# Performance work log

Measured on AMD Instinct MI355X. Metric: run time of the kernel, lower is better.

Reference implementation:

```python
import jax, jax.numpy as jnp
import numpy as np

B, S, D_MODEL, N_HEADS = 4, 2048, 1024, 16
HEAD_DIM = D_MODEL // N_HEADS


def setup_inputs() -> dict:
    key = jax.random.key(0)
    k_x, k_wqkv, k_bqkv, k_wout, k_bout = jax.random.split(key, 5)
    x = jax.random.normal(k_x, (B, S, D_MODEL), dtype=jnp.float32)
    # causal mask: True = masked (matches masked_fill semantics)
    mask = jnp.triu(jnp.ones((S, S), dtype=bool), k=1)[None, None, :, :]
    sc = 1.0 / np.sqrt(D_MODEL)
    w_qkv = jax.random.normal(k_wqkv, (3 * D_MODEL, D_MODEL), dtype=jnp.float32) * sc
    b_qkv = jax.random.normal(k_bqkv, (3 * D_MODEL,), dtype=jnp.float32) * 0.02
    w_out = jax.random.normal(k_wout, (D_MODEL, D_MODEL), dtype=jnp.float32) * sc
    b_out = jax.random.normal(k_bout, (D_MODEL,), dtype=jnp.float32) * 0.02
    return {"x": x, "mask": mask, "w_qkv": w_qkv, "b_qkv": b_qkv,
            "w_out": w_out, "b_out": b_out}


def reference(x, mask, w_qkv, b_qkv, w_out, b_out):
    b, s, d = x.shape
    qkv = x @ w_qkv.T + b_qkv                      # [B,S,3*D]
    qkv = qkv.reshape(b, s, 3, N_HEADS, HEAD_DIM)
    q = qkv[:, :, 0].transpose(0, 2, 1, 3)         # [B,H,S,Dh]
    k = qkv[:, :, 1].transpose(0, 2, 1, 3)
    v = qkv[:, :, 2].transpose(0, 2, 1, 3)
    scores = jnp.einsum('bhqd,bhkd->bhqk', q, k) / np.sqrt(HEAD_DIM)
    scores = jnp.where(mask, -jnp.inf, scores)
    attn = jax.nn.softmax(scores, axis=-1)         # dropout p=0.0 -> identity
    ctx = jnp.einsum('bhqk,bhkd->bhqd', attn, v)   # [B,H,S,Dh]
    ctx = ctx.transpose(0, 2, 1, 3).reshape(b, s, d)
    return ctx @ w_out.T + b_out
```

## Files before the change

kernel.cpp:

```cpp
#include <hip/hip_runtime.h>
#include <stdint.h>

typedef __attribute__((ext_vector_type(8))) short bf16x8;
typedef __attribute__((ext_vector_type(4))) float f32x4;
typedef unsigned short u16;

#define NUM_B 4
#define SEQ   2048
#define DM    1024
#define NH    16
#define DH    64
#define M_TOT (NUM_B * SEQ)

__device__ __forceinline__ float bf2f(u16 u) {
    union { unsigned int i; float f; } c; c.i = ((unsigned int)u) << 16; return c.f;
}
__device__ __forceinline__ u16 f2bf(float f) {
    union { float f; unsigned int i; } c; c.f = f;
    unsigned int u = c.i;
    return (u16)((u + 0x7FFFu + ((u >> 16) & 1u)) >> 16);
}
__device__ __forceinline__ unsigned int pack2(float a, float b) {
    return (unsigned int)f2bf(a) | ((unsigned int)f2bf(b) << 16);
}

#if __has_builtin(__builtin_amdgcn_exp2f)
#define EXP2F __builtin_amdgcn_exp2f
#else
#define EXP2F exp2f
#endif

#define GLOAD_LDS16(g, l)                                                     \
    __builtin_amdgcn_global_load_lds(                                         \
        (const __attribute__((address_space(1))) void*)(g),                   \
        (__attribute__((address_space(3))) void*)(l), 16, 0, 0)

__global__ void detect_dtype(const u16* __restrict__ x, int* __restrict__ flag) {
    __shared__ int cnt;
    if (threadIdx.x == 0) cnt = 0;
    __syncthreads();
    int local = 0;
    for (int i = threadIdx.x; i < 4096; i += 256) {
        const u16 v = x[i];
        const int e = (v >> 7) & 0xFF;
        if (v == 0 || (e >= 110 && e <= 145)) local++;
    }
    atomicAdd(&cnt, local);
    __syncthreads();
    if (threadIdx.x == 0) *flag = (cnt >= 3686) ? 0 : 1;
}

__global__ void convert_bf16(const void* __restrict__ in, u16* __restrict__ out,
                             long n, const int* __restrict__ flag)
{
    const long i0 = ((long)blockIdx.x * 256 + threadIdx.x) * 8;
    const long stride = (long)gridDim.x * 256 * 8;
    if (*flag) {
        const float* f = (const float*)in;
        for (long i = i0; i < n; i += stride) {
            float4 a = *(const float4*)(f + i);
            float4 b = *(const float4*)(f + i + 4);
            uint4 o;
            o.x = pack2(a.x, a.y); o.y = pack2(a.z, a.w);
            o.z = pack2(b.x, b.y); o.w = pack2(b.z, b.w);
            *(uint4*)(out + i) = o;
        }
    } else {
        const uint4* s = (const uint4*)in;
        for (long i = i0; i < n; i += stride)
            *(uint4*)(out + i) = s[i >> 3];
    }
}

template <int MODE, int N_TOT>
__global__ __launch_bounds__(256) void gemm_bt(
    const u16* __restrict__ A, const u16* __restrict__ Bm,
    const u16* __restrict__ bias,
    void* __restrict__ out0v, u16* __restrict__ out1, u16* __restrict__ out2,
    const int* __restrict__ outf32, long out_off)
{
    __shared__ __align__(16) u16 As[128 * 32];
    __shared__ __align__(16) u16 Bs[128 * 32];
    const int K = 1024;

    const int tid  = threadIdx.x;
    const int wave = tid >> 6;
    const int lane = tid & 63;
    const int l15  = lane & 15;
    const int quad = lane >> 4;

    const int m0 = blockIdx.y * 128;
    const int n0 = blockIdx.x * 128;
    const int wm = (wave >> 1) * 64;
    const int wn = (wave & 1) * 64;

    const int srow = lane >> 2;
    const int soff = (lane & 3) * 8;

    f32x4 acc[4][4];
#pragma unroll
    for (int i = 0; i < 4; ++i)
#pragma unroll
        for (int j = 0; j < 4; ++j)
            acc[i][j] = (f32x4){0.f, 0.f, 0.f, 0.f};

    for (int k0 = 0; k0 < K; k0 += 32) {
#pragma unroll
        for (int r = 0; r < 2; ++r) {
            const int chunk = wave * 2 + r;
            const int row   = chunk * 16 + srow;
            GLOAD_LDS16(&A[(size_t)(m0 + row) * K + k0 + soff], &As[chunk * 512]);
            GLOAD_LDS16(&Bm[(size_t)(n0 + row) * K + k0 + soff], &Bs[chunk * 512]);
        }
        __syncthreads();

        bf16x8 af[4], bfv[4];
#pragma unroll
        for (int i = 0; i < 4; ++i)
            af[i] = *(const bf16x8*)(&As[(wm + i * 16 + l15) * 32 + quad * 8]);
#pragma unroll
        for (int j = 0; j < 4; ++j)
            bfv[j] = *(const bf16x8*)(&Bs[(wn + j * 16 + l15) * 32 + quad * 8]);

#pragma unroll
        for (int i = 0; i < 4; ++i)
#pragma unroll
            for (int j = 0; j < 4; ++j)
                acc[i][j] = __builtin_amdgcn_mfma_f32_16x16x32_bf16(
                    af[i], bfv[j], acc[i][j], 0, 0, 0);
        __syncthreads();
    }

    const int of32 = outf32 ? *outf32 : 0;
#pragma unroll
    for (int j = 0; j < 4; ++j) {
        const int n  = n0 + wn + j * 16 + l15;
        const float bv = bf2f(bias[n]);
#pragma unroll
        for (int i = 0; i < 4; ++i) {
#pragma unroll
            for (int reg = 0; reg < 4; ++reg) {
                const int m = m0 + wm + i * 16 + quad * 4 + reg;
                const float v = acc[i][j][reg] + bv;
                if (MODE == 0) {
                    const int sel = n >> 10;
                    const int h   = (n >> 6) & 15;
                    const int dh  = n & 63;
                    const int b   = m >> 11;
                    const int s   = m & 2047;
                    if (sel == 2) {
                        out2[((size_t)((b * NH + h) * DH + dh)) * SEQ + s] = f2bf(v);
                    } else {
                        u16* dst = (sel == 0) ? (u16*)out0v : out1;
                        dst[((size_t)((b * NH + h) * SEQ + s)) * DH + dh] = f2bf(v);
                    }
                } else {
                    if (of32)
                        ((float*)out0v)[out_off + (size_t)m * N_TOT + n] = v;
                    else
                        ((u16*)out0v)[out_off + (size_t)m * N_TOT + n] = f2bf(v);
                }
            }
        }
    }
}

__global__ __launch_bounds__(256) void attn_fwd(
    const u16* __restrict__ Qb, const u16* __restrict__ Kb,
    const u16* __restrict__ Vt, u16* __restrict__ ctx)
{
    __shared__ __align__(16) u16 Ks[2][2048];
    __shared__ __align__(16) u16 Vs[2][2048];
    __shared__ __align__(16) short Pbuf[4][2][16 * 40];

    const int tid  = threadIdx.x;
    const int wave = tid >> 6;
    const int lane = tid & 63;
    const int l15  = lane & 15;
    const int quad = lane >> 4;

    const int bh = blockIdx.x;
    const int ya = blockIdx.y & 3, yk = blockIdx.y >> 2;
    const int yb = (yk == 0) ? ya : (yk == 1) ? 7 - ya : (yk == 2) ? 8 + ya : 15 - ya;

    const int q0 = yb * 128;
    const int qrowA = q0 + wave * 32;
    const size_t base  = (size_t)bh * SEQ * DH;
    const size_t baseT = (size_t)bh * DH * SEQ;
    const float sc_l2e = 0.18033688011112042f;

    bf16x8 qf[2][2];
#pragma unroll
    for (int f = 0; f < 2; ++f)
#pragma unroll
        for (int c = 0; c < 2; ++c)
            qf[f][c] = *(const bf16x8*)(&Qb[base + (size_t)(qrowA + f * 16 + l15) * DH + c * 32 + quad * 8]);

    f32x4 acc[2][4];
#pragma unroll
    for (int f = 0; f < 2; ++f)
#pragma unroll
        for (int j = 0; j < 4; ++j) acc[f][j] = (f32x4){0.f, 0.f, 0.f, 0.f};
    float lsum[2][4] = {{0.f, 0.f, 0.f, 0.f}, {0.f, 0.f, 0.f, 0.f}};

    const int ktend = yb * 4 + 3;
    const int mkt   = yb * 4 + wave;

    const int k_r = (wave & 1) * 16 + l15;
    const int k_c = ((wave >> 1) * 4 + quad) * 8;
    const int v_dh = wave * 16 + l15;
    const int v_k  = quad * 8;

    {
        GLOAD_LDS16(&Kb[base + (size_t)k_r * DH + k_c], &Ks[0][wave * 512]);
        GLOAD_LDS16(&Vt[baseT + (size_t)v_dh * SEQ + v_k], &Vs[0][wave * 512]);
    }

    for (int kt = 0; kt <= ktend; ++kt) {
        const int cur = kt & 1;
        __syncthreads();

        if (kt + 1 <= ktend) {
            const int nk0 = (kt + 1) * 32;
            GLOAD_LDS16(&Kb[base + (size_t)(nk0 + k_r) * DH + k_c],
                        &Ks[1 - cur][wave * 512]);
            GLOAD_LDS16(&Vt[baseT + (size_t)v_dh * SEQ + nk0 + v_k],
                        &Vs[1 - cur][wave * 512]);
        }

        if (kt <= mkt) {
            bf16x8 kf[2][2], vfr[4];
#pragma unroll
            for (int half = 0; half < 2; ++half)
#pragma unroll
                for (int c = 0; c < 2; ++c)
                    kf[half][c] = *(const bf16x8*)(&Ks[cur][(c * 2 + half) * 512 + lane * 8]);
#pragma unroll
            for (int j = 0; j < 4; ++j)
                vfr[j] = *(const bf16x8*)(&Vs[cur][j * 512 + lane * 8]);

            const int diag = (kt == mkt);
#pragma unroll
            for (int f = 0; f < 2; ++f) {
                f32x4 sc0 = (f32x4){0.f, 0.f, 0.f, 0.f};
                f32x4 sc1 = (f32x4){0.f, 0.f, 0.f, 0.f};
                sc0 = __builtin_amdgcn_mfma_f32_16x16x32_bf16(qf[f][0], kf[0][0], sc0, 0, 0, 0);
                sc0 = __builtin_amdgcn_mfma_f32_16x16x32_bf16(qf[f][1], kf[0][1], sc0, 0, 0, 0);
                sc1 = __builtin_amdgcn_mfma_f32_16x16x32_bf16(qf[f][0], kf[1][0], sc1, 0, 0, 0);
                sc1 = __builtin_amdgcn_mfma_f32_16x16x32_bf16(qf[f][1], kf[1][1], sc1, 0, 0, 0);

                float pa[4], pb[4];
                if (diag) {
#pragma unroll
                    for (int r = 0; r < 4; ++r) {
                        const int rr = quad * 4 + r;
                        if (f == 0) {
                            pa[r] = (l15 <= rr) ? EXP2F(sc0[r] * sc_l2e) : 0.f;
                            pb[r] = 0.f;
                        } else {
                            pa[r] = EXP2F(sc0[r] * sc_l2e);
                            pb[r] = (l15 <= rr) ? EXP2F(sc1[r] * sc_l2e) : 0.f;
                        }
                    }
                } else {
#pragma unroll
                    for (int r = 0; r < 4; ++r) {
                        pa[r] = EXP2F(sc0[r] * sc_l2e);
                        pb[r] = EXP2F(sc1[r] * sc_l2e);
                    }
                }
#pragma unroll
                for (int r = 0; r < 4; ++r)
                    lsum[f][r] += pa[r] + pb[r];

                short* pw = Pbuf[wave][f];
                asm volatile("" ::: "memory");
#pragma unroll
                for (int r = 0; r < 4; ++r) {
                    const int row = quad * 4 + r;
                    pw[row * 40 + l15]      = (short)f2bf(pa[r]);
                    pw[row * 40 + 16 + l15] = (short)f2bf(pb[r]);
                }
                asm volatile("" ::: "memory");
                const bf16x8 pf = *(const bf16x8*)(&pw[l15 * 40 + quad * 8]);

#pragma unroll
                for (int j = 0; j < 4; ++j)
                    acc[f][j] = __builtin_amdgcn_mfma_f32_16x16x32_bf16(pf, vfr[j], acc[f][j], 0, 0, 0);
            }
        }
    }

#pragma unroll
    for (int off = 1; off <= 8; off <<= 1)
#pragma unroll
        for (int f = 0; f < 2; ++f)
#pragma unroll
            for (int r = 0; r < 4; ++r)
                lsum[f][r] += __shfl_xor(lsum[f][r], off);

    const int b = bh >> 4;
    const int h = bh & 15;
#pragma unroll
    for (int f = 0; f < 2; ++f) {
#pragma unroll
        for (int r = 0; r < 4; ++r) {
            const float invL = 1.0f / lsum[f][r];
            const int qrow = qrowA + f * 16 + quad * 4 + r;
            const size_t rowaddr = ((size_t)(b * SEQ + qrow)) * DM + h * DH;
#pragma unroll
            for (int j = 0; j < 4; ++j)
                ctx[rowaddr + j * 16 + l15] = f2bf(acc[f][j][r] * invL);
        }
    }
}

extern "C" void kernel_launch(void* const* d_in, const int* in_sizes, int n_in,
                              void* d_out, int out_size, void* d_ws, size_t ws_size,
                              hipStream_t stream)
{
    auto find = [&](long want, int fb) -> const void* {
        for (int i = 0; i < n_in; ++i)
            if ((long)in_sizes[i] == want) return d_in[i];
        if (fb >= n_in) fb = n_in - 1;
        return d_in[fb];
    };
    const void* x     = find(8388608, 0);
    const void* w_qkv = find(3145728, 2);
    const void* b_qkv = find(3072,    3);
    const void* w_out = find(1048576, 4);
    const void* b_out = find(1024,    5);

    char* ws   = (char*)d_ws;
    int*  flag = (int*)ws;
    char* p    = ws + 256;

    u16* xbf    = (u16*)p;                 p += (size_t)8388608 * 2;
    u16* wqkvbf = (u16*)p;                 p += (size_t)3145728 * 2;
    u16* bqkvbf = (u16*)p;                 p += 8192;
    u16* woutbf = (u16*)p;                 p += (size_t)1048576 * 2;
    u16* boutbf = (u16*)p;                 p += 8192;

    const size_t tensor_bytes = (size_t)M_TOT * DM * sizeof(u16);
    const size_t chunk_bytes  = tensor_bytes / NUM_B;
    const size_t conv_end     = (size_t)(p - ws);

    detect_dtype<<<1, 256, 0, stream>>>((const u16*)x, flag);
    auto cgrid = [](long n) { long g = (n / 8 + 255) / 256; return (int)(g > 2048 ? 2048 : g); };
    convert_bf16<<<cgrid(8388608), 256, 0, stream>>>(x,     xbf,    8388608, flag);
    convert_bf16<<<cgrid(3145728), 256, 0, stream>>>(w_qkv, wqkvbf, 3145728, flag);
    convert_bf16<<<cgrid(3072),    256, 0, stream>>>(b_qkv, bqkvbf, 3072,    flag);
    convert_bf16<<<cgrid(1048576), 256, 0, stream>>>(w_out, woutbf, 1048576, flag);
    convert_bf16<<<cgrid(1024),    256, 0, stream>>>(b_out, boutbf, 1024,    flag);

    if (ws_size >= conv_end + 4 * tensor_bytes) {
        u16* Qb  = (u16*)(ws + conv_end);
        u16* Kb  = (u16*)(ws + conv_end + tensor_bytes);
        u16* Vb  = (u16*)(ws + conv_end + 2 * tensor_bytes);
        u16* ctx = (u16*)(ws + conv_end + 3 * tensor_bytes);

        gemm_bt<0, 3072><<<dim3(24, 64), 256, 0, stream>>>(
            xbf, wqkvbf, bqkvbf, Qb, Kb, Vb, nullptr, 0);
        attn_fwd<<<dim3(NUM_B * NH, SEQ / 128), 256, 0, stream>>>(Qb, Kb, Vb, ctx);
        gemm_bt<1, 1024><<<dim3(8, 64), 256, 0, stream>>>(
            ctx, woutbf, boutbf, d_out, nullptr, nullptr, flag, 0);
    } else {
        u16* Qb  = (u16*)(ws + conv_end);
        u16* Kb  = (u16*)(ws + conv_end + chunk_bytes);
        u16* Vb  = (u16*)(ws + conv_end + 2 * chunk_bytes);
        u16* ctx = (u16*)(ws + conv_end + 3 * chunk_bytes);
        for (int b = 0; b < NUM_B; ++b) {
            const long eoff = (long)b * SEQ * DM;
            gemm_bt<0, 3072><<<dim3(24, 16), 256, 0, stream>>>(
                xbf + eoff, wqkvbf, bqkvbf, Qb, Kb, Vb, nullptr, 0);
            attn_fwd<<<dim3(NH, SEQ / 128), 256, 0, stream>>>(Qb, Kb, Vb, ctx);
            gemm_bt<1, 1024><<<dim3(8, 16), 256, 0, stream>>>(
                ctx, woutbf, boutbf, d_out, nullptr, nullptr, flag, eoff);
        }
    }
}
```

Before: 327.9 us.

## Double-buffer LDS tiles in bf16 GEMM to overlap loads with MFMA

Shared-memory A/B tiles in the GEMM kernel become double-buffered. The next K-slice is prefetched into the alternate buffer right after the barrier, so global-to-LDS copies run while MFMAs consume the current buffer. This drops one of the two barriers per iteration. The cost is doubled LDS use per block, which may lower occupancy.

```diff
diff --git a/kernel.cpp b/kernel.cpp
--- a/kernel.cpp
+++ b/kernel.cpp
@@ -79,8 +79,8 @@
     void* __restrict__ out0v, u16* __restrict__ out1, u16* __restrict__ out2,
     const int* __restrict__ outf32, long out_off)
 {
-    __shared__ __align__(16) u16 As[128 * 32];
-    __shared__ __align__(16) u16 Bs[128 * 32];
+    __shared__ __align__(16) u16 As[2][128 * 32];
+    __shared__ __align__(16) u16 Bs[2][128 * 32];
     const int K = 1024;
 
     const int tid  = threadIdx.x;
@@ -97,6 +97,10 @@
     const int srow = lane >> 2;
     const int soff = (lane & 3) * 8;
 
+    const int chunk0 = wave * 2;
+    const int row0   = chunk0 * 16 + srow;
+    const int row1   = row0 + 16;
+
     f32x4 acc[4][4];
 #pragma unroll
     for (int i = 0; i < 4; ++i)
@@ -104,23 +108,32 @@
         for (int j = 0; j < 4; ++j)
             acc[i][j] = (f32x4){0.f, 0.f, 0.f, 0.f};
 
-    for (int k0 = 0; k0 < K; k0 += 32) {
-#pragma unroll
-        for (int r = 0; r < 2; ++r) {
-            const int chunk = wave * 2 + r;
-            const int row   = chunk * 16 + srow;
-            GLOAD_LDS16(&A[(size_t)(m0 + row) * K + k0 + soff], &As[chunk * 512]);
-            GLOAD_LDS16(&Bm[(size_t)(n0 + row) * K + k0 + soff], &Bs[chunk * 512]);
-        }
+    {
+        GLOAD_LDS16(&A[(size_t)(m0 + row0) * K + soff], &As[0][chunk0 * 512]);
+        GLOAD_LDS16(&Bm[(size_t)(n0 + row0) * K + soff], &Bs[0][chunk0 * 512]);
+        GLOAD_LDS16(&A[(size_t)(m0 + row1) * K + soff], &As[0][(chunk0 + 1) * 512]);
+        GLOAD_LDS16(&Bm[(size_t)(n0 + row1) * K + soff], &Bs[0][(chunk0 + 1) * 512]);
+    }
+
+    int buf = 0;
+    for (int k0 = 0; k0 < K; k0 += 32, buf ^= 1) {
         __syncthreads();
 
+        if (k0 + 32 < K) {
+            const int kn = k0 + 32;
+            GLOAD_LDS16(&A[(size_t)(m0 + row0) * K + kn + soff], &As[buf ^ 1][chunk0 * 512]);
+            GLOAD_LDS16(&Bm[(size_t)(n0 + row0) * K + kn + soff], &Bs[buf ^ 1][chunk0 * 512]);
+            GLOAD_LDS16(&A[(size_t)(m0 + row1) * K + kn + soff], &As[buf ^ 1][(chunk0 + 1) * 512]);
+            GLOAD_LDS16(&Bm[(size_t)(n0 + row1) * K + kn + soff], &Bs[buf ^ 1][(chunk0 + 1) * 512]);
+        }
+
         bf16x8 af[4], bfv[4];
 #pragma unroll
         for (int i = 0; i < 4; ++i)
-            af[i] = *(const bf16x8*)(&As[(wm + i * 16 + l15) * 32 + quad * 8]);
+            af[i] = *(const bf16x8*)(&As[buf][(wm + i * 16 + l15) * 32 + quad * 8]);
 #pragma unroll
         for (int j = 0; j < 4; ++j)
-            bfv[j] = *(const bf16x8*)(&Bs[(wn + j * 16 + l15) * 32 + quad * 8]);
+            bfv[j] = *(const bf16x8*)(&Bs[buf][(wn + j * 16 + l15) * 32 + quad * 8]);
 
 #pragma unroll
         for (int i = 0; i < 4; ++i)
@@ -128,7 +141,6 @@
             for (int j = 0; j < 4; ++j)
                 acc[i][j] = __builtin_amdgcn_mfma_f32_16x16x32_bf16(
                     af[i], bfv[j], acc[i][j], 0, 0, 0);
-        __syncthreads();
     }
 
     const int of32 = outf32 ? *outf32 : 0;
```

Result: no change. 330.9 us (+0.9%).
